# Performance work log

Hardware: AMD Instinct MI355X
Metric: run time of the kernel (lower is better)

## Reference

```python
import jax, jax.numpy as jnp
import numpy as np

DEPTH, B, S, E, H, EXP = 6, 16, 511, 1024, 16, 2
HD = E // H
FF = EXP * E


def _layernorm(x, g, b, eps=1e-5):
    m = jnp.mean(x, axis=-1, keepdims=True)
    v = jnp.var(x, axis=-1, keepdims=True)
    return (x - m) * jax.lax.rsqrt(v + eps) * g + b


def setup_inputs() -> dict:
    key = jax.random.key(0)
    ks = jax.random.split(key, 12)
    sc = 0.02
    inp = {
        "x": jax.random.normal(ks[0], (B, S, E), jnp.float32),
        "cls_token": jax.random.normal(ks[1], (1, 1, E), jnp.float32),
        "pos_emb": jax.random.normal(ks[2], (1, S + 1, E), jnp.float32),
        # attention projections (bias=False in source), stacked over depth
        "Wq": jax.random.normal(ks[3], (DEPTH, E, E), jnp.float32) * sc,
        "Wk": jax.random.normal(ks[4], (DEPTH, E, E), jnp.float32) * sc,
        "Wv": jax.random.normal(ks[5], (DEPTH, E, E), jnp.float32) * sc,
        "Wp": jax.random.normal(ks[6], (DEPTH, E, E), jnp.float32) * sc,
        # layernorm params
        "ln1_g": jnp.ones((DEPTH, E), jnp.float32),
        "ln1_b": jnp.zeros((DEPTH, E), jnp.float32),
        "ln2_g": jnp.ones((DEPTH, E), jnp.float32),
        "ln2_b": jnp.zeros((DEPTH, E), jnp.float32),
        # feed-forward (with bias, as nn.Linear default)
        "W1": jax.random.normal(ks[7], (DEPTH, E, FF), jnp.float32) * sc,
        "b1": jnp.zeros((DEPTH, FF), jnp.float32),
        "W2": jax.random.normal(ks[8], (DEPTH, FF, E), jnp.float32) * sc,
        "b2": jnp.zeros((DEPTH, E), jnp.float32),
    }
    return inp


def reference(x, cls_token, pos_emb, Wq, Wk, Wv, Wp,
              ln1_g, ln1_b, ln2_g, ln2_b, W1, b1, W2, b2):
    b = x.shape[0]
    # AddClsToken + PositionalEmbedding
    h = jnp.concatenate([jnp.broadcast_to(cls_token, (b, 1, E)), x], axis=1) + pos_emb
    scale = jnp.asarray(E ** 0.5, h.dtype)  # source scales by sqrt(emb_size)
    for i in range(DEPTH):
        # --- self-attention sublayer (pre-LN) ---
        res = h
        xn = _layernorm(h, ln1_g[i], ln1_b[i])
        q = (xn @ Wq[i]).reshape(b, -1, H, HD).transpose(0, 2, 1, 3)  # b h n d
        k = (xn @ Wk[i]).reshape(b, -1, H, HD).transpose(0, 2, 1, 3)
        v = (xn @ Wv[i]).reshape(b, -1, H, HD).transpose(0, 2, 1, 3)
        energy = jnp.einsum('bhqd,bhkd->bhqk', q, k)
        att = jax.nn.softmax(energy / scale, axis=-1)
        out = jnp.einsum('bhqk,bhkd->bhqd', att, v)
        out = out.transpose(0, 2, 1, 3).reshape(b, -1, E)
        h = out @ Wp[i] + res
        # --- feed-forward sublayer (pre-LN) ---
        res = h
        yn = _layernorm(h, ln2_g[i], ln2_b[i])
        ff = jax.nn.gelu(yn @ W1[i] + b1[i], approximate=False) @ W2[i] + b2[i]
        h = ff + res
    return h
```

## Files before the change

kernel.cpp:

```cpp
#include <hip/hip_runtime.h>
#include <cstdint>
#include <cstddef>

#define DEPTH 6
#define NB    16
#define NSEQ  512
#define EMB   1024
#define NHEAD 16
#define HDIM  64
#define FFD   2048
#define NTOK  (NB * NSEQ)

typedef unsigned short u16;
using bf16x8 = __attribute__((ext_vector_type(8))) __bf16;
using f32x4  = __attribute__((ext_vector_type(4))) float;
using u16x4  = __attribute__((ext_vector_type(4))) u16;
using u16x8  = __attribute__((ext_vector_type(8))) u16;

typedef __attribute__((address_space(1))) uint32_t* as1_u32p;
typedef __attribute__((address_space(3))) uint32_t* as3_u32p;
typedef __attribute__((address_space(3))) u16*      as3_u16p;

__device__ __forceinline__ u16 f2bf(float f) {
  union { float f; uint32_t u; } v; v.f = f;
  uint32_t u = v.u;
  return (u16)((u + 0x7FFFu + ((u >> 16) & 1u)) >> 16);
}

__device__ __forceinline__ void gload_lds16(const u16* g, u16* l) {
  void* gp = const_cast<u16*>(g);
  __builtin_amdgcn_global_load_lds((as1_u32p)gp, (as3_u32p)l, 16, 0, 0);
}

template<int ROWBYTES>
__device__ __forceinline__ void stage16k(const u16* g0, int ldk, u16* lds) {
  int t = threadIdx.x;
#pragma unroll
  for (int i = 0; i < 4; ++i) {
    int off = (i * 256 + t) * 16;
    int row = off / ROWBYTES;
    int pc  = (off % ROWBYTES) >> 4;
    int lc  = pc ^ (row & 7);
    gload_lds16(g0 + (size_t)row * ldk + lc * 8, lds + (off >> 1));
  }
}

__global__ __launch_bounds__(256)
void wprep_k(const float* __restrict__ W, u16* __restrict__ Wt,
             int K, int N, size_t inL, size_t outL, size_t outOff)
{
  int ntiles = N >> 6, ktiles = K >> 6;
  int bid = blockIdx.x;
  int l = bid / (ktiles * ntiles);
  int r = bid % (ktiles * ntiles);
  int kt = r / ntiles, nt = r % ntiles;
  const float* in = W + (size_t)l * inL + (size_t)(kt * 64) * N + nt * 64;
  u16* out = Wt + (size_t)l * outL + outOff + (size_t)(nt * 64) * K + kt * 64;
  __shared__ float tile[64][65];
  int t = threadIdx.x;
  int tr = t >> 4, tc = (t & 15) * 4;
#pragma unroll
  for (int i = 0; i < 4; ++i) {
    f32x4 v = *(const f32x4*)(in + (size_t)(tr + i * 16) * N + tc);
    tile[tr + i * 16][tc + 0] = v[0];
    tile[tr + i * 16][tc + 1] = v[1];
    tile[tr + i * 16][tc + 2] = v[2];
    tile[tr + i * 16][tc + 3] = v[3];
  }
  __syncthreads();
#pragma unroll
  for (int i = 0; i < 4; ++i) {
    int nr = tr + i * 16;
    u16x4 o;
    o[0] = f2bf(tile[tc + 0][nr]);
    o[1] = f2bf(tile[tc + 1][nr]);
    o[2] = f2bf(tile[tc + 2][nr]);
    o[3] = f2bf(tile[tc + 3][nr]);
    *(u16x4*)(out + (size_t)nr * K + tc) = o;
  }
}

__global__ __launch_bounds__(256)
void embed_k(const float* __restrict__ x, const float* __restrict__ cls,
             const float* __restrict__ pos, float* __restrict__ H)
{
  int row = blockIdx.x, t = threadIdx.x;
  int b_ = row >> 9, n = row & 511;
  int c = t * 4;
  f32x4 p = *(const f32x4*)(pos + (size_t)n * EMB + c);
  f32x4 s;
  if (n == 0) s = *(const f32x4*)(cls + c);
  else        s = *(const f32x4*)(x + ((size_t)b_ * 511 + (n - 1)) * EMB + c);
  f32x4 o = s + p;
  *(f32x4*)(H + (size_t)row * EMB + c) = o;
}

__global__ __launch_bounds__(256)
void ln_k(const float* __restrict__ H, const float* __restrict__ g,
          const float* __restrict__ b, u16* __restrict__ out)
{
  int row = blockIdx.x, t = threadIdx.x;
  const float* hp = H + (size_t)row * EMB;
  f32x4 v = *(const f32x4*)(hp + t * 4);
  float s  = v[0] + v[1] + v[2] + v[3];
  float ss = v[0]*v[0] + v[1]*v[1] + v[2]*v[2] + v[3]*v[3];
#pragma unroll
  for (int m = 1; m <= 32; m <<= 1) { s += __shfl_xor(s, m); ss += __shfl_xor(ss, m); }
  __shared__ float red[8];
  if ((t & 63) == 0) { red[(t >> 6) * 2] = s; red[(t >> 6) * 2 + 1] = ss; }
  __syncthreads();
  float S  = red[0] + red[2] + red[4] + red[6];
  float SS = red[1] + red[3] + red[5] + red[7];
  float mean = S * (1.0f / EMB);
  float var  = SS * (1.0f / EMB) - mean * mean;
  float rs = rsqrtf(var + 1e-5f);
  f32x4 gg = *(const f32x4*)(g + t * 4);
  f32x4 bb = *(const f32x4*)(b + t * 4);
  u16x4 o;
#pragma unroll
  for (int i = 0; i < 4; ++i) o[i] = f2bf((v[i] - mean) * rs * gg[i] + bb[i]);
  *(u16x4*)(out + (size_t)row * EMB + t * 4) = o;
}

template<int EPI>
__global__ __launch_bounds__(256, 3)
void gemm_k(const u16* __restrict__ A, const u16* __restrict__ Bt,
            int nbn, int K,
            const float* __restrict__ bias, float* __restrict__ H,
            u16* __restrict__ outB,
            u16* __restrict__ qo, u16* __restrict__ ko, u16* __restrict__ vto)
{
  __shared__ u16 sm[16384];
  int cpx = gridDim.x >> 3;
  int logical = (blockIdx.x & 7) * cpx + (blockIdx.x >> 3);
  int bm = logical / nbn, bn = logical % nbn;
  int t = threadIdx.x, lane = t & 63, w = t >> 6;
  int wm = w >> 1, wn = w & 1;
  const u16* Ab = A  + (size_t)(bm * 128) * K;
  const u16* Bb = Bt + (size_t)(bn * 128) * K;
  int nkt = K >> 6;

  const f32x4 vzero = {0.f, 0.f, 0.f, 0.f};
  f32x4 acc[4][4];
#pragma unroll
  for (int i = 0; i < 4; ++i)
#pragma unroll
    for (int j = 0; j < 4; ++j) acc[i][j] = vzero;

  int r0 = lane & 15;
  int hi = lane >> 4;
  int kk0 = hi * 8;

  for (int kt = 0; kt < nkt; ++kt) {
    stage16k<128>(Ab + kt * 64, K, sm);
    stage16k<128>(Bb + kt * 64, K, sm + 8192);
    __syncthreads();
    const char* smAp = (const char*)sm;
    const char* smBp = (const char*)(sm + 8192);
#pragma unroll
    for (int ks = 0; ks < 2; ++ks) {
      int kk = ks * 32 + kk0;
      bf16x8 a[4], b[4];
#pragma unroll
      for (int mf = 0; mf < 4; ++mf) {
        int row = wm * 64 + mf * 16 + r0;
        a[mf] = *(const bf16x8*)(smAp + row * 128 + ((kk * 2) ^ ((row & 7) << 4)));
      }
#pragma unroll
      for (int nf = 0; nf < 4; ++nf) {
        int row = wn * 64 + nf * 16 + r0;
        b[nf] = *(const bf16x8*)(smBp + row * 128 + ((kk * 2) ^ ((row & 7) << 4)));
      }
#pragma unroll
      for (int mf = 0; mf < 4; ++mf)
#pragma unroll
        for (int nf = 0; nf < 4; ++nf)
          acc[mf][nf] = __builtin_amdgcn_mfma_f32_16x16x32_bf16(a[mf], b[nf], acc[mf][nf], 0, 0, 0);
    }
    __syncthreads();
  }

  if (EPI == 1 || EPI == 3) {
    int m0 = bm * 128 + wm * 64;
    int n0 = bn * 128 + wn * 64;
#pragma unroll
    for (int mf = 0; mf < 4; ++mf) {
#pragma unroll
      for (int nf = 0; nf < 4; ++nf) {
        int col  = n0 + nf * 16 + r0;
        int rowb = m0 + mf * 16 + hi * 4;
#pragma unroll
        for (int j = 0; j < 4; ++j) {
          float v = acc[mf][nf][j];
          size_t idx = (size_t)(rowb + j) * EMB + col;
          if (EPI == 1) H[idx] = v + H[idx];
          else          H[idx] = v + bias[col] + H[idx];
        }
      }
    }
    return;
  }

  int sec = (bn * 128) >> 10;
  bool vsec = (EPI == 0) && (sec == 2);
#pragma unroll
  for (int mf = 0; mf < 4; ++mf) {
#pragma unroll
    for (int nf = 0; nf < 4; ++nf) {
      int colL = wn * 64 + nf * 16 + r0;
#pragma unroll
      for (int j = 0; j < 4; ++j) {
        int rowL = wm * 64 + mf * 16 + hi * 4 + j;
        float v = acc[mf][nf][j];
        if (EPI == 2) {
          float xg = v + bias[bn * 128 + colL];
          v = 0.5f * xg * (1.0f + erff(xg * 0.70710678118654752f));
        }
        u16 o = f2bf(v);
        if (!vsec)
          sm[rowL * 128 + (colL & 7) + ((((colL >> 3) ^ (rowL & 7))) << 3)] = o;
        else
          sm[colL * 128 + (rowL & 7) + ((((rowL >> 3) ^ (colL & 7))) << 3)] = o;
      }
    }
  }
  __syncthreads();

  int c  = t & 15;
  int rb = t >> 4;
  if (!vsec) {
#pragma unroll
    for (int i = 0; i < 8; ++i) {
      int row = rb * 8 + i;
      u16x8 v = *(const u16x8*)(sm + row * 128 + ((c ^ (row & 7)) << 3));
      if (EPI == 2) {
        int rowg = bm * 128 + row;
        int colg = bn * 128 + c * 8;
        *(u16x8*)(outB + (size_t)rowg * FFD + colg) = v;
      } else {
        int n_ = bm * 128 + row;
        int b_ = n_ >> 9, tok = n_ & 511;
        int c0 = (bn * 128 - sec * 1024) + c * 8;
        int hh = c0 >> 6, d0 = c0 & 63;
        u16* dst = (sec == 0) ? qo : ko;
        *(u16x8*)(dst + (((size_t)(b_ * NHEAD + hh) * NSEQ + tok) * HDIM) + d0) = v;
      }
    }
  } else {
#pragma unroll
    for (int i = 0; i < 8; ++i) {
      int rowp = rb * 8 + i;
      u16x8 v = *(const u16x8*)(sm + rowp * 128 + ((c ^ (rowp & 7)) << 3));
      int c0 = (bn * 128 - 2048) + rowp;
      int hh = c0 >> 6, d = c0 & 63;
      int tok0 = bm * 128 + c * 8;
      int b_ = tok0 >> 9;
      *(u16x8*)(vto + ((size_t)(b_ * NHEAD + hh) * HDIM + d) * NSEQ + (tok0 & 511)) = v;
    }
  }
}

__global__ __launch_bounds__(256, 2)
void attn_k(const u16* __restrict__ Q, const u16* __restrict__ Kk,
            const u16* __restrict__ Vt, u16* __restrict__ AO)
{
  __shared__ u16 kvS[32768];
  __shared__ u16 Pt[4][2048];
  int bid = blockIdx.x;
  int bh = (bid & 7) * 32 + (bid >> 6);
  int qt = (bid >> 3) & 7;
  int t = threadIdx.x, lane = t & 63, w = t >> 6;
  const u16* Kb = Kk + (size_t)bh * (NSEQ * HDIM);
  const u16* Vb = Vt + (size_t)bh * (HDIM * NSEQ);
  int r0 = lane & 15, hi = lane >> 4, kk0 = hi * 8;

  int qrow = qt * 64 + w * 16 + r0;
  const u16* Qp = Q + ((size_t)bh * NSEQ + qrow) * HDIM;
  bf16x8 qf0 = *(const bf16x8*)(Qp + kk0);
  bf16x8 qf1 = *(const bf16x8*)(Qp + 32 + kk0);

  const f32x4 vzero = {0.f, 0.f, 0.f, 0.f};
  f32x4 accS[32];
#pragma unroll
  for (int f = 0; f < 32; ++f) accS[f] = vzero;

#pragma unroll
  for (int i = 0; i < 4; ++i)
    stage16k<128>(Kb + (size_t)i * 128 * HDIM, HDIM, kvS + i * 8192);
  __syncthreads();

  const char* smK = (const char*)kvS;
#pragma unroll
  for (int kf = 0; kf < 32; ++kf) {
    int krow = kf * 16 + r0;
    int swz = (krow & 7) << 4;
    bf16x8 b0 = *(const bf16x8*)(smK + krow * 128 + (((kk0)      * 2) ^ swz));
    bf16x8 b1 = *(const bf16x8*)(smK + krow * 128 + (((32 + kk0) * 2) ^ swz));
    accS[kf] = __builtin_amdgcn_mfma_f32_16x16x32_bf16(qf0, b0, accS[kf], 0, 0, 0);
    accS[kf] = __builtin_amdgcn_mfma_f32_16x16x32_bf16(qf1, b1, accS[kf], 0, 0, 0);
  }
  __syncthreads();

#pragma unroll
  for (int i = 0; i < 4; ++i)
    stage16k<1024>(Vb + (size_t)i * 16 * NSEQ, NSEQ, kvS + i * 8192);

  float mx[4], den[4], rden[4];
#pragma unroll
  for (int j = 0; j < 4; ++j) {
    float m = -1e30f;
#pragma unroll
    for (int f = 0; f < 32; ++f) m = fmaxf(m, accS[f][j]);
    m = fmaxf(m, __shfl_xor(m, 1));
    m = fmaxf(m, __shfl_xor(m, 2));
    m = fmaxf(m, __shfl_xor(m, 4));
    m = fmaxf(m, __shfl_xor(m, 8));
    mx[j] = m;
    den[j] = 0.f;
  }
  uint32_t pb[64];
#pragma unroll
  for (int f = 0; f < 32; ++f) {
    float p0 = __expf((accS[f][0] - mx[0]) * 0.03125f);
    float p1 = __expf((accS[f][1] - mx[1]) * 0.03125f);
    float p2 = __expf((accS[f][2] - mx[2]) * 0.03125f);
    float p3 = __expf((accS[f][3] - mx[3]) * 0.03125f);
    den[0] += p0; den[1] += p1; den[2] += p2; den[3] += p3;
    pb[f * 2 + 0] = (uint32_t)f2bf(p0) | ((uint32_t)f2bf(p1) << 16);
    pb[f * 2 + 1] = (uint32_t)f2bf(p2) | ((uint32_t)f2bf(p3) << 16);
  }
#pragma unroll
  for (int j = 0; j < 4; ++j) {
    float d = den[j];
    d += __shfl_xor(d, 1); d += __shfl_xor(d, 2);
    d += __shfl_xor(d, 4); d += __shfl_xor(d, 8);
    rden[j] = 1.0f / d;
  }
  __syncthreads();

  int perm0 = ((r0 & 4) << 2) + ((r0 >> 3) << 2) + (r0 & 3);
  uint32_t ptb = (uint32_t)(uintptr_t)(as3_u16p)&Pt[w][0];
  uint32_t trBase = ptb + r0 * 2 + hi * 128;
  char* PtW = (char*)&Pt[w][0];
  const char* smV = (const char*)kvS;

  f32x4 accO[4];
#pragma unroll
  for (int nf = 0; nf < 4; ++nf) accO[nf] = vzero;

#pragma unroll
  for (int kt = 0; kt < 4; ++kt) {
#pragma unroll
    for (int fl = 0; fl < 8; ++fl) {
      int f = kt * 8 + fl;
      int row = (fl >> 1) * 32 + perm0 + ((fl & 1) << 3);
      *(uint2*)(PtW + row * 32 + hi * 8) = make_uint2(pb[f * 2], pb[f * 2 + 1]);
    }
    asm volatile("s_waitcnt lgkmcnt(0)" ::: "memory");
    __builtin_amdgcn_sched_barrier(0);
#pragma unroll
    for (int s = 0; s < 4; ++s) {
      uint2 t0, t1;
      uint32_t a0 = trBase + s * 1024;
      asm volatile("ds_read_b64_tr_b16 %0, %1" : "=v"(t0) : "v"(a0) : "memory");
      asm volatile("ds_read_b64_tr_b16 %0, %1" : "=v"(t1) : "v"(a0 + 512) : "memory");
      bf16x8 vb[4];
      int kkv = kt * 128 + s * 32 + kk0;
#pragma unroll
      for (int nf = 0; nf < 4; ++nf) {
        int d = nf * 16 + r0;
        vb[nf] = *(const bf16x8*)(smV + d * 1024 + ((kkv * 2) ^ ((d & 7) << 4)));
      }
      asm volatile("s_waitcnt lgkmcnt(0)" ::: "memory");
      __builtin_amdgcn_sched_barrier(0);
      union { uint4 u; bf16x8 v; } pa;
      pa.u = make_uint4(t0.x, t0.y, t1.x, t1.y);
#pragma unroll
      for (int nf = 0; nf < 4; ++nf)
        accO[nf] = __builtin_amdgcn_mfma_f32_16x16x32_bf16(pa.v, vb[nf], accO[nf], 0, 0, 0);
    }
  }

  int b_ = bh >> 4, hh = bh & 15;
#pragma unroll
  for (int nf = 0; nf < 4; ++nf)
#pragma unroll
    for (int j = 0; j < 4; ++j) {
      int ql = hi * 4 + j;
      int tok = qt * 64 + w * 16 + ql;
      int col = hh * 64 + nf * 16 + r0;
      AO[((size_t)(b_ * NSEQ + tok)) * EMB + col] = f2bf(accO[nf][j] * rden[j]);
    }
}

extern "C" void kernel_launch(void* const* d_in, const int* in_sizes, int n_in,
                              void* d_out, int out_size, void* d_ws, size_t ws_size,
                              hipStream_t stream)
{
  const float* x    = (const float*)d_in[0];
  const float* cls  = (const float*)d_in[1];
  const float* pos  = (const float*)d_in[2];
  const float* Wq   = (const float*)d_in[3];
  const float* Wk   = (const float*)d_in[4];
  const float* Wv   = (const float*)d_in[5];
  const float* Wp   = (const float*)d_in[6];
  const float* ln1g = (const float*)d_in[7];
  const float* ln1b = (const float*)d_in[8];
  const float* ln2g = (const float*)d_in[9];
  const float* ln2b = (const float*)d_in[10];
  const float* W1   = (const float*)d_in[11];
  const float* b1   = (const float*)d_in[12];
  const float* W2   = (const float*)d_in[13];
  const float* b2   = (const float*)d_in[14];
  float* H = (float*)d_out;

  char* ws = (char*)d_ws;
  u16* wqkv = (u16*)(ws + 0);
  u16* wp   = (u16*)(ws + 37748736);
  u16* w1t  = (u16*)(ws + 50331648);
  u16* w2t  = (u16*)(ws + 75497472);
  u16* xn   = (u16*)(ws + 100663296);
  u16* qb   = (u16*)(ws + 117440512);
  u16* kb   = (u16*)(ws + 134217728);
  u16* vtb  = (u16*)(ws + 150994944);
  u16* ffb  = qb;

  wprep_k<<<1536, 256, 0, stream>>>(Wq, wqkv, 1024, 1024, 1048576, 3145728, 0);
  wprep_k<<<1536, 256, 0, stream>>>(Wk, wqkv, 1024, 1024, 1048576, 3145728, 1048576);
  wprep_k<<<1536, 256, 0, stream>>>(Wv, wqkv, 1024, 1024, 1048576, 3145728, 2097152);
  wprep_k<<<1536, 256, 0, stream>>>(Wp, wp,   1024, 1024, 1048576, 1048576, 0);
  wprep_k<<<3072, 256, 0, stream>>>(W1, w1t,  1024, 2048, 2097152, 2097152, 0);
  wprep_k<<<3072, 256, 0, stream>>>(W2, w2t,  2048, 1024, 2097152, 2097152, 0);

  embed_k<<<NTOK, 256, 0, stream>>>(x, cls, pos, H);

  for (int l = 0; l < DEPTH; ++l) {
    ln_k<<<NTOK, 256, 0, stream>>>(H, ln1g + l * EMB, ln1b + l * EMB, xn);
    gemm_k<0><<<64 * 24, 256, 0, stream>>>(xn, wqkv + (size_t)l * 3145728, 24, 1024,
                                           nullptr, nullptr, nullptr, qb, kb, vtb);
    attn_k<<<2048, 256, 0, stream>>>(qb, kb, vtb, xn);
    gemm_k<1><<<64 * 8, 256, 0, stream>>>(xn, wp + (size_t)l * 1048576, 8, 1024,
                                          nullptr, H, nullptr, nullptr, nullptr, nullptr);
    ln_k<<<NTOK, 256, 0, stream>>>(H, ln2g + l * EMB, ln2b + l * EMB, xn);
    gemm_k<2><<<64 * 16, 256, 0, stream>>>(xn, w1t + (size_t)l * 2097152, 16, 1024,
                                           b1 + l * FFD, nullptr, ffb, nullptr, nullptr, nullptr);
    gemm_k<3><<<64 * 8, 256, 0, stream>>>(ffb, w2t + (size_t)l * 2097152, 8, 2048,
                                          b2 + l * EMB, H, nullptr, nullptr, nullptr, nullptr);
  }
}
```

Measured before the change: 1.525 ms.

## Rewrite attention as flash-style online softmax with double-buffered K/V and 32x32 MFMA

The attention kernel is restructured into an online-softmax loop over four 128-key chunks. K and V chunks are double-buffered in LDS so the next chunk loads while the current one is computed. It switches to 32x32x16 MFMA with S computed transposed, so probabilities stay in registers and are packed through v_cvt_pk_bf16 and permlane32 swaps instead of an LDS round trip with transposed reads. Each block now handles 128 queries (1024 blocks instead of 2048), with less LDS and fewer barriers. In exchange it adds rescaling work per chunk and may lower occupancy and parallelism.

```diff
diff --git a/kernel.cpp b/kernel.cpp
--- a/kernel.cpp
+++ b/kernel.cpp
@@ -14,12 +14,12 @@
 typedef unsigned short u16;
 using bf16x8 = __attribute__((ext_vector_type(8))) __bf16;
 using f32x4  = __attribute__((ext_vector_type(4))) float;
+using f32x16 = __attribute__((ext_vector_type(16))) float;
 using u16x4  = __attribute__((ext_vector_type(4))) u16;
 using u16x8  = __attribute__((ext_vector_type(8))) u16;
 
 typedef __attribute__((address_space(1))) uint32_t* as1_u32p;
 typedef __attribute__((address_space(3))) uint32_t* as3_u32p;
-typedef __attribute__((address_space(3))) u16*      as3_u16p;
 
 __device__ __forceinline__ u16 f2bf(float f) {
   union { float f; uint32_t u; } v; v.f = f;
@@ -264,133 +264,111 @@
 void attn_k(const u16* __restrict__ Q, const u16* __restrict__ Kk,
             const u16* __restrict__ Vt, u16* __restrict__ AO)
 {
-  __shared__ u16 kvS[32768];
-  __shared__ u16 Pt[4][2048];
+  __shared__ u16 bufK[2][8192];
+  __shared__ u16 bufV[2][8192];
   int bid = blockIdx.x;
-  int bh = (bid & 7) * 32 + (bid >> 6);
-  int qt = (bid >> 3) & 7;
+  int logical = (bid & 7) * 128 + (bid >> 3);
+  int bh = logical >> 2, qt = logical & 3;
   int t = threadIdx.x, lane = t & 63, w = t >> 6;
+  int l31 = lane & 31, hi32 = lane >> 5;
   const u16* Kb = Kk + (size_t)bh * (NSEQ * HDIM);
   const u16* Vb = Vt + (size_t)bh * (HDIM * NSEQ);
-  int r0 = lane & 15, hi = lane >> 4, kk0 = hi * 8;
-
-  int qrow = qt * 64 + w * 16 + r0;
-  const u16* Qp = Q + ((size_t)bh * NSEQ + qrow) * HDIM;
-  bf16x8 qf0 = *(const bf16x8*)(Qp + kk0);
-  bf16x8 qf1 = *(const bf16x8*)(Qp + 32 + kk0);
-
-  const f32x4 vzero = {0.f, 0.f, 0.f, 0.f};
-  f32x4 accS[32];
-#pragma unroll
-  for (int f = 0; f < 32; ++f) accS[f] = vzero;
-
-#pragma unroll
-  for (int i = 0; i < 4; ++i)
-    stage16k<128>(Kb + (size_t)i * 128 * HDIM, HDIM, kvS + i * 8192);
+
+  int qbase = qt * 128 + w * 32;
+  const u16* Qp = Q + ((size_t)bh * NSEQ + qbase + l31) * HDIM;
+  bf16x8 qf[4];
+#pragma unroll
+  for (int tk = 0; tk < 4; ++tk)
+    qf[tk] = *(const bf16x8*)(Qp + 16 * tk + 8 * hi32);
+
+  stage16k<128>(Kb, HDIM, &bufK[0][0]);
+  stage16k<256>(Vb, NSEQ, &bufV[0][0]);
   __syncthreads();
 
-  const char* smK = (const char*)kvS;
-#pragma unroll
-  for (int kf = 0; kf < 32; ++kf) {
-    int krow = kf * 16 + r0;
-    int swz = (krow & 7) << 4;
-    bf16x8 b0 = *(const bf16x8*)(smK + krow * 128 + (((kk0)      * 2) ^ swz));
-    bf16x8 b1 = *(const bf16x8*)(smK + krow * 128 + (((32 + kk0) * 2) ^ swz));
-    accS[kf] = __builtin_amdgcn_mfma_f32_16x16x32_bf16(qf0, b0, accS[kf], 0, 0, 0);
-    accS[kf] = __builtin_amdgcn_mfma_f32_16x16x32_bf16(qf1, b1, accS[kf], 0, 0, 0);
-  }
-  __syncthreads();
-
-#pragma unroll
-  for (int i = 0; i < 4; ++i)
-    stage16k<1024>(Vb + (size_t)i * 16 * NSEQ, NSEQ, kvS + i * 8192);
-
-  float mx[4], den[4], rden[4];
-#pragma unroll
-  for (int j = 0; j < 4; ++j) {
-    float m = -1e30f;
-#pragma unroll
-    for (int f = 0; f < 32; ++f) m = fmaxf(m, accS[f][j]);
-    m = fmaxf(m, __shfl_xor(m, 1));
-    m = fmaxf(m, __shfl_xor(m, 2));
-    m = fmaxf(m, __shfl_xor(m, 4));
-    m = fmaxf(m, __shfl_xor(m, 8));
-    mx[j] = m;
-    den[j] = 0.f;
-  }
-  uint32_t pb[64];
-#pragma unroll
-  for (int f = 0; f < 32; ++f) {
-    float p0 = __expf((accS[f][0] - mx[0]) * 0.03125f);
-    float p1 = __expf((accS[f][1] - mx[1]) * 0.03125f);
-    float p2 = __expf((accS[f][2] - mx[2]) * 0.03125f);
-    float p3 = __expf((accS[f][3] - mx[3]) * 0.03125f);
-    den[0] += p0; den[1] += p1; den[2] += p2; den[3] += p3;
-    pb[f * 2 + 0] = (uint32_t)f2bf(p0) | ((uint32_t)f2bf(p1) << 16);
-    pb[f * 2 + 1] = (uint32_t)f2bf(p2) | ((uint32_t)f2bf(p3) << 16);
-  }
-#pragma unroll
-  for (int j = 0; j < 4; ++j) {
-    float d = den[j];
-    d += __shfl_xor(d, 1); d += __shfl_xor(d, 2);
-    d += __shfl_xor(d, 4); d += __shfl_xor(d, 8);
-    rden[j] = 1.0f / d;
-  }
-  __syncthreads();
-
-  int perm0 = ((r0 & 4) << 2) + ((r0 >> 3) << 2) + (r0 & 3);
-  uint32_t ptb = (uint32_t)(uintptr_t)(as3_u16p)&Pt[w][0];
-  uint32_t trBase = ptb + r0 * 2 + hi * 128;
-  char* PtW = (char*)&Pt[w][0];
-  const char* smV = (const char*)kvS;
-
-  f32x4 accO[4];
-#pragma unroll
-  for (int nf = 0; nf < 4; ++nf) accO[nf] = vzero;
-
-#pragma unroll
-  for (int kt = 0; kt < 4; ++kt) {
-#pragma unroll
-    for (int fl = 0; fl < 8; ++fl) {
-      int f = kt * 8 + fl;
-      int row = (fl >> 1) * 32 + perm0 + ((fl & 1) << 3);
-      *(uint2*)(PtW + row * 32 + hi * 8) = make_uint2(pb[f * 2], pb[f * 2 + 1]);
-    }
-    asm volatile("s_waitcnt lgkmcnt(0)" ::: "memory");
-    __builtin_amdgcn_sched_barrier(0);
-#pragma unroll
-    for (int s = 0; s < 4; ++s) {
-      uint2 t0, t1;
-      uint32_t a0 = trBase + s * 1024;
-      asm volatile("ds_read_b64_tr_b16 %0, %1" : "=v"(t0) : "v"(a0) : "memory");
-      asm volatile("ds_read_b64_tr_b16 %0, %1" : "=v"(t1) : "v"(a0 + 512) : "memory");
-      bf16x8 vb[4];
-      int kkv = kt * 128 + s * 32 + kk0;
-#pragma unroll
-      for (int nf = 0; nf < 4; ++nf) {
-        int d = nf * 16 + r0;
-        vb[nf] = *(const bf16x8*)(smV + d * 1024 + ((kkv * 2) ^ ((d & 7) << 4)));
-      }
-      asm volatile("s_waitcnt lgkmcnt(0)" ::: "memory");
-      __builtin_amdgcn_sched_barrier(0);
+  f32x16 accO[2];
+#pragma unroll
+  for (int r = 0; r < 16; ++r) { accO[0][r] = 0.f; accO[1][r] = 0.f; }
+  float m_run = -1e30f, den = 0.f;
+  const float inv32 = 0.03125f;
+
+  for (int c = 0; c < 4; ++c) {
+    if (c < 3) {
+      stage16k<128>(Kb + (size_t)(c + 1) * 128 * HDIM, HDIM, &bufK[(c + 1) & 1][0]);
+      stage16k<256>(Vb + (c + 1) * 128, NSEQ, &bufV[(c + 1) & 1][0]);
+    }
+    const char* smK = (const char*)&bufK[c & 1][0];
+    f32x16 s[4];
+#pragma unroll
+    for (int kt = 0; kt < 4; ++kt) {
+#pragma unroll
+      for (int r = 0; r < 16; ++r) s[kt][r] = 0.f;
+#pragma unroll
+      for (int tk = 0; tk < 4; ++tk) {
+        int row = kt * 32 + l31;
+        bf16x8 kf = *(const bf16x8*)(smK + row * 128 +
+                      ((32 * tk + 16 * hi32) ^ ((row & 7) << 4)));
+        s[kt] = __builtin_amdgcn_mfma_f32_32x32x16_bf16(kf, qf[tk], s[kt], 0, 0, 0);
+      }
+    }
+    float mc = -1e30f;
+#pragma unroll
+    for (int kt = 0; kt < 4; ++kt)
+#pragma unroll
+      for (int r = 0; r < 16; ++r) mc = fmaxf(mc, s[kt][r]);
+    mc = fmaxf(mc, __shfl_xor(mc, 32));
+    float newm = fmaxf(m_run, mc);
+    float fac = __expf((m_run - newm) * inv32);
+    den *= fac;
+#pragma unroll
+    for (int r = 0; r < 16; ++r) { accO[0][r] *= fac; accO[1][r] *= fac; }
+    m_run = newm;
+#pragma unroll
+    for (int kt = 0; kt < 4; ++kt)
+#pragma unroll
+      for (int r = 0; r < 16; ++r) {
+        float p = __expf((s[kt][r] - newm) * inv32);
+        den += p;
+        s[kt][r] = p;
+      }
+    uint32_t pb[32];
+#pragma unroll
+    for (int j = 0; j < 32; ++j) {
+      float lo = s[j >> 3][(2 * j) & 15];
+      float hi = s[j >> 3][((2 * j) & 15) + 1];
+      asm("v_cvt_pk_bf16_f32 %0, %1, %2" : "=v"(pb[j]) : "v"(lo), "v"(hi));
+    }
+    const char* smV = (const char*)&bufV[c & 1][0];
+#pragma unroll
+    for (int ks = 0; ks < 8; ++ks) {
+      uint32_t x0 = pb[4 * ks], y0 = pb[4 * ks + 2];
+      uint32_t x1 = pb[4 * ks + 1], y1 = pb[4 * ks + 3];
+      asm("v_permlane32_swap_b32 %0, %1" : "+v"(x0), "+v"(y0));
+      asm("v_permlane32_swap_b32 %0, %1" : "+v"(x1), "+v"(y1));
       union { uint4 u; bf16x8 v; } pa;
-      pa.u = make_uint4(t0.x, t0.y, t1.x, t1.y);
-#pragma unroll
-      for (int nf = 0; nf < 4; ++nf)
-        accO[nf] = __builtin_amdgcn_mfma_f32_16x16x32_bf16(pa.v, vb[nf], accO[nf], 0, 0, 0);
-    }
-  }
-
+      pa.u = make_uint4(x0, x1, y0, y1);
+#pragma unroll
+      for (int dt = 0; dt < 2; ++dt) {
+        int row = dt * 32 + l31;
+        bf16x8 vb = *(const bf16x8*)(smV + row * 256 +
+                      ((32 * ks + 16 * hi32) ^ ((row & 7) << 4)));
+        accO[dt] = __builtin_amdgcn_mfma_f32_32x32x16_bf16(pa.v, vb, accO[dt], 0, 0, 0);
+      }
+    }
+    __syncthreads();
+  }
+
+  float denf = den + __shfl_xor(den, 32);
+  float rden = 1.0f / denf;
   int b_ = bh >> 4, hh = bh & 15;
 #pragma unroll
-  for (int nf = 0; nf < 4; ++nf)
-#pragma unroll
-    for (int j = 0; j < 4; ++j) {
-      int ql = hi * 4 + j;
-      int tok = qt * 64 + w * 16 + ql;
-      int col = hh * 64 + nf * 16 + r0;
-      AO[((size_t)(b_ * NSEQ + tok)) * EMB + col] = f2bf(accO[nf][j] * rden[j]);
-    }
+  for (int r = 0; r < 16; ++r) {
+    int qoff = (r & 3) + 8 * (r >> 2) + 4 * hi32;
+    float rd = __shfl(rden, qoff);
+    int tok = qbase + qoff;
+    size_t base = ((size_t)(b_ * NSEQ + tok)) * EMB + hh * 64 + l31;
+    AO[base]      = f2bf(accO[0][r] * rd);
+    AO[base + 32] = f2bf(accO[1][r] * rd);
+  }
 }
 
 extern "C" void kernel_launch(void* const* d_in, const int* in_sizes, int n_in,
@@ -438,7 +416,7 @@
     ln_k<<<NTOK, 256, 0, stream>>>(H, ln1g + l * EMB, ln1b + l * EMB, xn);
     gemm_k<0><<<64 * 24, 256, 0, stream>>>(xn, wqkv + (size_t)l * 3145728, 24, 1024,
                                            nullptr, nullptr, nullptr, qb, kb, vtb);
-    attn_k<<<2048, 256, 0, stream>>>(qb, kb, vtb, xn);
+    attn_k<<<1024, 256, 0, stream>>>(qb, kb, vtb, xn);
     gemm_k<1><<<64 * 8, 256, 0, stream>>>(xn, wp + (size_t)l * 1048576, 8, 1024,
                                           nullptr, H, nullptr, nullptr, nullptr, nullptr);
     ln_k<<<NTOK, 256, 0, stream>>>(H, ln2g + l * EMB, ln2b + l * EMB, xn);
```

Measured after the change: 1.453 ms. 1.05x faster.
